# Kernel tuning notes

Hardware: AMD Instinct MI355X
Metric: run time of the kernel (lower is better)

Reference implementation:

```python
import jax, jax.numpy as jnp
import numpy as np

N_NODES = 20000
N_EDGES = 320000
F_IN = 256      # num_features_mol
HIDDEN = 512    # hidden_size


def _glorot(key, shape):
    fan_in, fan_out = shape
    lim = jnp.sqrt(6.0 / (fan_in + fan_out)).astype(jnp.float32)
    return jax.random.uniform(key, shape, jnp.float32, -lim, lim)


def setup_inputs() -> dict:
    key = jax.random.key(0)
    ks = jax.random.split(key, 12)
    x = jax.random.normal(ks[0], (N_NODES, F_IN), jnp.float32)
    edge_index = jax.random.randint(ks[1], (2, N_EDGES), 0, N_NODES, dtype=jnp.int64)
    d1, d2, d3 = F_IN * 2, F_IN * 2, F_IN * 4  # 512, 512, 1024
    return {
        "x": x,
        "edge_index": edge_index,
        # SAGEConv layer i: lin_l (neighbor, with bias), lin_r (root, no bias)
        "Wl1": _glorot(ks[2], (F_IN, d1)), "bl1": jnp.zeros((d1,), jnp.float32),
        "Wr1": _glorot(ks[3], (F_IN, d1)),
        "Wl2": _glorot(ks[4], (d1, d2)), "bl2": jnp.zeros((d2,), jnp.float32),
        "Wr2": _glorot(ks[5], (d1, d2)),
        "Wl3": _glorot(ks[6], (d2, d3)), "bl3": jnp.zeros((d3,), jnp.float32),
        "Wr3": _glorot(ks[7], (d2, d3)),
        # mol_fc_g1: Linear(4*F -> hidden)
        "Wfc": _glorot(ks[8], (d3, HIDDEN)), "bfc": jnp.zeros((HIDDEN,), jnp.float32),
    }


def _sage_mean(x, src, dst, Wl, bl, Wr):
    # mean-aggregate neighbor features: messages flow src -> dst
    msg = x[src]                                               # [E, d]
    agg = jax.ops.segment_sum(msg, dst, num_segments=N_NODES)  # [N, d]
    cnt = jax.ops.segment_sum(jnp.ones((src.shape[0],), x.dtype), dst,
                              num_segments=N_NODES)            # [N]
    mean = agg / jnp.maximum(cnt, 1.0)[:, None]                # zero-deg -> 0
    return mean @ Wl + bl + x @ Wr


def reference(x, edge_index, Wl1, bl1, Wr1, Wl2, bl2, Wr2, Wl3, bl3, Wr3, Wfc, bfc):
    src, dst = edge_index[0], edge_index[1]
    h = jax.nn.relu(_sage_mean(x, src, dst, Wl1, bl1, Wr1))
    h = jax.nn.relu(_sage_mean(h, src, dst, Wl2, bl2, Wr2))
    h = jax.nn.relu(_sage_mean(h, src, dst, Wl3, bl3, Wr3))
    return h @ Wfc + bfc                                       # [N, HIDDEN]
```

## Files before the change

### kernel.cpp

```cpp
#include <hip/hip_runtime.h>
#include <hip/hip_bf16.h>


typedef __bf16 bf16x8 __attribute__((ext_vector_type(8)));
typedef float  f32x4  __attribute__((ext_vector_type(4)));

#define N_NODES 20000
#define N_EDGES 320000
#define MPAD 20096

__device__ __forceinline__ int clampi(int v, int lo, int hi) {
    return v < lo ? lo : (v > hi ? hi : v);
}

__device__ __forceinline__ void load16_lds(const void* g, void* l) {
    __builtin_amdgcn_global_load_lds(
        (const __attribute__((address_space(1))) void*)g,
        (__attribute__((address_space(3))) void*)l, 16, 0, 0);
}


struct TDesc { const float* W; __bf16* Wt; int K, N, KT, koff, tile0; };
struct TDescs { TDesc d[7]; };

__global__ void k_prep(TDescs ds, const float* __restrict__ x,
                       __bf16* __restrict__ xrm, __bf16* __restrict__ acat,
                       const int* __restrict__ ei, int* __restrict__ cnt) {
    __shared__ float tile[32][33];
    int b = blockIdx.x;
    int tid = threadIdx.y * 32 + threadIdx.x;

    if (b < 2304) {
        int di = 0;
#pragma unroll
        for (int i = 1; i < 7; ++i)
            if (b >= ds.d[i].tile0) di = i;
        const float* W = ds.d[di].W;
        __bf16* Wt = ds.d[di].Wt;
        int N = ds.d[di].N, KT = ds.d[di].KT, koff = ds.d[di].koff;
        int t = b - ds.d[di].tile0;
        int ntn = N >> 5;
        int nb = (t % ntn) * 32, kb = (t / ntn) * 32;
        for (int i = 0; i < 32; i += 8) {
            int k = kb + threadIdx.y + i, n = nb + threadIdx.x;
            tile[threadIdx.y + i][threadIdx.x] = W[(size_t)k * N + n];
        }
        __syncthreads();
        for (int i = 0; i < 32; i += 8) {
            int n = nb + threadIdx.y + i, k = koff + kb + threadIdx.x;
            size_t o = (size_t)(n >> 7) * ((size_t)KT * 128) + (size_t)(k >> 3) * 1024 +
                       (size_t)((n & 127) * 8) + (k & 7);
            Wt[o] = (__bf16)tile[threadIdx.x][threadIdx.y + i];
        }
    } else if (b < 4804) {
        int node = (b - 2304) * 8 + (tid >> 5);
        int f0 = (tid & 31) * 8;
        float4 u = *(const float4*)(x + (size_t)node * 256 + f0);
        float4 w = *(const float4*)(x + (size_t)node * 256 + f0 + 4);
        alignas(16) __bf16 tmp[8] = {(__bf16)u.x, (__bf16)u.y, (__bf16)u.z, (__bf16)u.w,
                                     (__bf16)w.x, (__bf16)w.y, (__bf16)w.z, (__bf16)w.w};
        *(uint4*)(xrm + (size_t)node * 256 + f0) = *(const uint4*)tmp;
        *(uint4*)(acat + (size_t)(node >> 7) * (512 * 128) +
                  (size_t)(32 + (f0 >> 3)) * 1024 + (size_t)((node & 127) * 8)) =
            *(const uint4*)tmp;
    } else {
        int e = (b - 4804) * 256 + tid;
        atomicAdd(&cnt[clampi(ei[N_EDGES + e], 0, N_NODES - 1)], 1);
    }
}


__global__ __launch_bounds__(1024) void k_scan(const int* __restrict__ cnt,
                                               int* __restrict__ off,
                                               int* __restrict__ cur, int n) {
    __shared__ int sm[1024];
    __shared__ int carry;
    int tid = threadIdx.x;
    if (tid == 0) carry = 0;
    __syncthreads();
    for (int base = 0; base < n; base += 1024) {
        int i = base + tid;
        int v = (i < n) ? cnt[i] : 0;
        sm[tid] = v;
        __syncthreads();
        for (int s = 1; s < 1024; s <<= 1) {
            int t = (tid >= s) ? sm[tid - s] : 0;
            __syncthreads();
            sm[tid] += t;
            __syncthreads();
        }
        int exc = carry + sm[tid] - v;
        if (i < n) { off[i] = exc; cur[i] = exc; }
        __syncthreads();
        if (tid == 1023) carry += sm[1023];
        __syncthreads();
    }
    if (tid == 0) off[n] = carry;
}

__global__ void k_fill(const int* __restrict__ ei, int E,
                       int* __restrict__ cur, int* __restrict__ csr) {
    int e = blockIdx.x * blockDim.x + threadIdx.x;
    if (e < E) {
        int dst = clampi(ei[E + e], 0, N_NODES - 1);
        int src = clampi(ei[e], 0, N_NODES - 1);
        int pos = atomicAdd(&cur[dst], 1);
        if (pos >= 0 && pos < E) csr[pos] = src;
    }
}


template <int D, int KC>
__global__ __launch_bounds__(256) void k_agg(const __hip_bfloat16* __restrict__ hrm,
                                             const int* __restrict__ off,
                                             const int* __restrict__ csr,
                                             __bf16* __restrict__ acat) {
    constexpr int FPL = D / 64;
    int wave = threadIdx.x >> 6, lane = threadIdx.x & 63;
    int node = blockIdx.x * 4 + wave;
    int c0 = lane * FPL;
    int beg = off[node], end = off[node + 1];
    float a[FPL] = {};

    if constexpr (FPL == 8) {
        auto ldrow = [&](int s) { return *(const uint4*)(hrm + (size_t)s * D + c0); };
        auto addv = [&](uint4 v) {
            const __hip_bfloat16* hb = (const __hip_bfloat16*)&v;
#pragma unroll
            for (int j = 0; j < 8; ++j) a[j] += __bfloat162float(hb[j]);
        };
        int e = beg;
        for (; e + 3 < end; e += 4) {
            int s0 = csr[e], s1 = csr[e + 1], s2 = csr[e + 2], s3 = csr[e + 3];
            uint4 v0 = ldrow(s0), v1 = ldrow(s1), v2 = ldrow(s2), v3 = ldrow(s3);
            addv(v0); addv(v1); addv(v2); addv(v3);
        }
        for (; e < end; ++e) addv(ldrow(csr[e]));
    } else {
        auto ldrow = [&](int s) { return *(const uint2*)(hrm + (size_t)s * D + c0); };
        auto addv = [&](uint2 v) {
            const __hip_bfloat16* hb = (const __hip_bfloat16*)&v;
#pragma unroll
            for (int j = 0; j < 4; ++j) a[j] += __bfloat162float(hb[j]);
        };
        int e = beg;
        for (; e + 3 < end; e += 4) {
            int s0 = csr[e], s1 = csr[e + 1], s2 = csr[e + 2], s3 = csr[e + 3];
            uint2 v0 = ldrow(s0), v1 = ldrow(s1), v2 = ldrow(s2), v3 = ldrow(s3);
            addv(v0); addv(v1); addv(v2); addv(v3);
        }
        for (; e < end; ++e) addv(ldrow(csr[e]));
    }

    float inv = 1.f / fmaxf((float)(end - beg), 1.f);
    alignas(16) __bf16 tmp[FPL];
#pragma unroll
    for (int j = 0; j < FPL; ++j) tmp[j] = (__bf16)(a[j] * inv);

    __bf16* base = acat + (size_t)(node >> 7) * ((size_t)KC * 128) +
                   (size_t)((node & 127) * 8);
    if constexpr (FPL == 8) {
        *(uint4*)(base + (size_t)lane * 1024) = *(const uint4*)tmp;
    } else {
        *(uint2*)(base + (size_t)(lane >> 1) * 1024 + (size_t)((lane & 1) * 4)) =
            *(const uint2*)tmp;
    }
}


template <bool RELU, int OUTMODE>
__global__ __launch_bounds__(256) void k_gemm(const __bf16* __restrict__ A, int K, int M,
                                              const __bf16* __restrict__ B,
                                              const float* __restrict__ bias,
                                              __bf16* __restrict__ osw, int Kc, int coff,
                                              __bf16* __restrict__ orm, int ldrm,
                                              float* __restrict__ of32, int ldf,
                                              int rtiles, int ctlog2) {
    constexpr int SMEM = (OUTMODE == 2) ? 34816 : 32768;
    __shared__ char smem[SMEM];
    __bf16* Alds = (__bf16*)smem;
    __bf16* Blds = (__bf16*)(smem + 16384);

    int bid = blockIdx.x;
    int xcd = bid & 7, local = bid >> 3;
    int cmask = (1 << ctlog2) - 1;
    int colTile = local & cmask;
    int rowTile = (local >> ctlog2) * 8 + xcd;
    if (rowTile >= rtiles) return;

    const __bf16* Atile = A + (size_t)rowTile * ((size_t)K * 128);
    const __bf16* Btile = B + (size_t)colTile * ((size_t)K * 128);

    int tid = threadIdx.x;
    int wave = tid >> 6, lane = tid & 63;
    int wr = wave >> 1, wc = wave & 1;
    int quad = lane >> 4, l16 = lane & 15;

    f32x4 acc[4][4] = {};

    for (int k0 = 0; k0 < K; k0 += 64) {
        __syncthreads();
        const __bf16* gA = Atile + (size_t)k0 * 128;
        const __bf16* gB = Btile + (size_t)k0 * 128;
#pragma unroll
        for (int j = 0; j < 4; ++j) {
            int slot = (j * 256 + tid) * 8;
            load16_lds(gA + slot, Alds + slot);
            load16_lds(gB + slot, Blds + slot);
        }
        __syncthreads();
#pragma unroll
        for (int sp = 0; sp < 2; ++sp) {
            bf16x8 af[4], bf[4];
#pragma unroll
            for (int mi = 0; mi < 4; ++mi)
                af[mi] = *(const bf16x8*)(Alds + sp * 4096 + quad * 1024 +
                                          (wr * 64 + mi * 16 + l16) * 8);
#pragma unroll
            for (int ni = 0; ni < 4; ++ni)
                bf[ni] = *(const bf16x8*)(Blds + sp * 4096 + quad * 1024 +
                                          (wc * 64 + ni * 16 + l16) * 8);
#pragma unroll
            for (int mi = 0; mi < 4; ++mi)
#pragma unroll
                for (int ni = 0; ni < 4; ++ni)
                    acc[mi][ni] = __builtin_amdgcn_mfma_f32_16x16x32_bf16(
                        af[mi], bf[ni], acc[mi][ni], 0, 0, 0);
        }
    }

    int col0 = colTile * 128;
    int row0 = rowTile * 128;
    __syncthreads();

    if (OUTMODE != 2) {
        __bf16* cb = (__bf16*)smem;
#pragma unroll
        for (int ni = 0; ni < 4; ++ni) {
            int ct = wc * 64 + ni * 16 + l16;
            float bv = bias[col0 + ct];
#pragma unroll
            for (int mi = 0; mi < 4; ++mi) {
                int rb = wr * 64 + mi * 16 + quad * 4;
#pragma unroll
                for (int r = 0; r < 4; ++r) {
                    float v = acc[mi][ni][r] + bv;
                    if (RELU) v = fmaxf(v, 0.f);
                    cb[(ct >> 3) * 1024 + (rb + r) * 8 + (ct & 7)] = (__bf16)v;
                }
            }
        }
        __syncthreads();
        __bf16* dst = osw + (size_t)rowTile * ((size_t)Kc * 128) +
                      (size_t)((coff + col0) >> 3) * 1024;
#pragma unroll
        for (int p2 = 0; p2 < 8; ++p2) {
            int idx = (p2 * 256 + tid) * 8;
            *(uint4*)(dst + idx) = *(const uint4*)(cb + idx);
        }
        if (OUTMODE == 1) {
#pragma unroll
            for (int p2 = 0; p2 < 8; ++p2) {
                int rr = p2 * 16 + (tid >> 4);
                int cc = tid & 15;
                *(uint4*)(orm + (size_t)(row0 + rr) * ldrm + col0 + cc * 8) =
                    *(const uint4*)(cb + cc * 1024 + rr * 8);
            }
        }
    } else {
        float* cf = (float*)smem;
#pragma unroll
        for (int h = 0; h < 2; ++h) {
            if (wc == h) {
#pragma unroll
                for (int ni = 0; ni < 4; ++ni) {
                    int ctl = ni * 16 + l16;
                    float bv = bias[col0 + h * 64 + ctl];
#pragma unroll
                    for (int mi = 0; mi < 4; ++mi) {
                        int rb = wr * 64 + mi * 16 + quad * 4;
#pragma unroll
                        for (int r = 0; r < 4; ++r) {
                            float v = acc[mi][ni][r] + bv;
                            if (RELU) v = fmaxf(v, 0.f);
                            cf[(rb + r) * 68 + ctl] = v;
                        }
                    }
                }
            }
            __syncthreads();
            int chunk = tid & 15, rl = tid >> 4;
#pragma unroll
            for (int p2 = 0; p2 < 8; ++p2) {
                int rt = p2 * 16 + rl;
                int row = row0 + rt;
                if (row < M) {
                    float4 v = *(const float4*)(cf + rt * 68 + chunk * 4);
                    *(float4*)(of32 + (size_t)row * ldf + col0 + h * 64 + chunk * 4) = v;
                }
            }
            __syncthreads();
        }
    }
}


extern "C" void kernel_launch(void* const* d_in, const int* in_sizes, int n_in,
                              void* d_out, int out_size, void* d_ws, size_t ws_size,
                              hipStream_t stream) {
    const float* x   = (const float*)d_in[0];
    const int*   ei  = (const int*)d_in[1];
    const float* Wl1 = (const float*)d_in[2];
    const float* bl1 = (const float*)d_in[3];
    const float* Wr1 = (const float*)d_in[4];
    const float* Wl2 = (const float*)d_in[5];
    const float* bl2 = (const float*)d_in[6];
    const float* Wr2 = (const float*)d_in[7];
    const float* Wl3 = (const float*)d_in[8];
    const float* bl3 = (const float*)d_in[9];
    const float* Wr3 = (const float*)d_in[10];
    const float* Wfc = (const float*)d_in[11];
    const float* bfc = (const float*)d_in[12];
    float* out = (float*)d_out;

    const int NN = N_NODES, E = N_EDGES;

    char* p = (char*)d_ws;
    auto alloc = [&](size_t bytes) {
        char* r = p;
        p += (bytes + 511) & ~(size_t)511;
        return r;
    };
    int* cnt   = (int*)alloc((size_t)NN * 4);
    int* off   = (int*)alloc((size_t)(NN + 1) * 4);
    int* cur   = (int*)alloc((size_t)NN * 4);
    int* csr   = (int*)alloc((size_t)E * 4);
    __bf16* Acat1 = (__bf16*)alloc((size_t)MPAD * 512 * 2);
    __bf16* Acat2 = (__bf16*)alloc((size_t)MPAD * 1024 * 2);
    __bf16* Acat3 = (__bf16*)alloc((size_t)MPAD * 1024 * 2);
    __bf16* Hrm   = (__bf16*)alloc((size_t)MPAD * 512 * 2);
    __bf16* Xrm   = (__bf16*)alloc((size_t)MPAD * 256 * 2);
    __bf16* Wt1 = (__bf16*)alloc((size_t)512 * 512 * 2);
    __bf16* Wt2 = (__bf16*)alloc((size_t)512 * 1024 * 2);
    __bf16* Wt3 = (__bf16*)alloc((size_t)1024 * 1024 * 2);
    __bf16* Wt4 = (__bf16*)alloc((size_t)512 * 1024 * 2);
    __bf16* H3 = Acat2;

    hipMemsetAsync(cnt, 0, (size_t)NN * 4, stream);
    TDescs td;
    td.d[0] = {Wl1, Wt1, 256, 512, 512, 0, 0};
    td.d[1] = {Wr1, Wt1, 256, 512, 512, 256, 128};
    td.d[2] = {Wl2, Wt2, 512, 512, 1024, 0, 256};
    td.d[3] = {Wr2, Wt2, 512, 512, 1024, 512, 512};
    td.d[4] = {Wl3, Wt3, 512, 1024, 1024, 0, 768};
    td.d[5] = {Wr3, Wt3, 512, 1024, 1024, 512, 1280};
    td.d[6] = {Wfc, Wt4, 1024, 512, 1024, 0, 1792};
    k_prep<<<6054, dim3(32, 8), 0, stream>>>(td, x, Xrm, Acat1, ei, cnt);

    k_scan<<<1, 1024, 0, stream>>>(cnt, off, cur, NN);
    k_fill<<<(E + 255) / 256, 256, 0, stream>>>(ei, E, cur, csr);

    int rtiles = (NN + 127) / 128;
    int rg = ((rtiles + 7) / 8) * 8;

    k_agg<256, 512><<<NN / 4, 256, 0, stream>>>(
        (const __hip_bfloat16*)Xrm, off, csr, Acat1);
    k_gemm<true, 1><<<rg * 4, 256, 0, stream>>>(
        Acat1, 512, NN, Wt1, bl1, Acat2, 1024, 512, Hrm, 512, nullptr, 0, rtiles, 2);

    k_agg<512, 1024><<<NN / 4, 256, 0, stream>>>(
        (const __hip_bfloat16*)Hrm, off, csr, Acat2);
    k_gemm<true, 1><<<rg * 4, 256, 0, stream>>>(
        Acat2, 1024, NN, Wt2, bl2, Acat3, 1024, 512, Hrm, 512, nullptr, 0, rtiles, 2);

    k_agg<512, 1024><<<NN / 4, 256, 0, stream>>>(
        (const __hip_bfloat16*)Hrm, off, csr, Acat3);
    k_gemm<true, 0><<<rg * 8, 256, 0, stream>>>(
        Acat3, 1024, NN, Wt3, bl3, H3, 1024, 0, nullptr, 0, nullptr, 0, rtiles, 3);

    k_gemm<false, 2><<<rg * 4, 256, 0, stream>>>(
        H3, 1024, NN, Wt4, bfc, nullptr, 0, 0, nullptr, 0, out, 512, rtiles, 2);
}
```

Baseline: 443.4 us.

## Double-buffer GEMM LDS tiles and parallelize CSR offset scan across blocks

The GEMM main loop now uses two LDS buffers, so the global-to-LDS load of the next K tile is issued while MFMAs run on the current one, and one barrier per iteration is dropped. The single-block serial prefix scan over node counts is replaced by a three-kernel scan: a per-block scan, a serial carry over about 20 block sums, and a carry add. Doubling shared memory to 64KB per block may cut GEMM occupancy, and the scan now costs two extra kernel launches.

```diff
diff --git a/kernel.cpp b/kernel.cpp
--- a/kernel.cpp
+++ b/kernel.cpp
@@ -70,32 +70,43 @@
 }
 
 
-__global__ __launch_bounds__(1024) void k_scan(const int* __restrict__ cnt,
-                                               int* __restrict__ off,
-                                               int* __restrict__ cur, int n) {
+__global__ __launch_bounds__(1024) void k_scan_block(const int* __restrict__ cnt,
+                                                     int* __restrict__ off,
+                                                     int* __restrict__ bsum, int n) {
     __shared__ int sm[1024];
-    __shared__ int carry;
-    int tid = threadIdx.x;
-    if (tid == 0) carry = 0;
+    int b = blockIdx.x, tid = threadIdx.x;
+    int i = b * 1024 + tid;
+    int v = (i < n) ? cnt[i] : 0;
+    sm[tid] = v;
     __syncthreads();
-    for (int base = 0; base < n; base += 1024) {
-        int i = base + tid;
-        int v = (i < n) ? cnt[i] : 0;
-        sm[tid] = v;
+    for (int s = 1; s < 1024; s <<= 1) {
+        int t = (tid >= s) ? sm[tid - s] : 0;
         __syncthreads();
-        for (int s = 1; s < 1024; s <<= 1) {
-            int t = (tid >= s) ? sm[tid - s] : 0;
-            __syncthreads();
-            sm[tid] += t;
-            __syncthreads();
-        }
-        int exc = carry + sm[tid] - v;
-        if (i < n) { off[i] = exc; cur[i] = exc; }
+        sm[tid] += t;
         __syncthreads();
-        if (tid == 1023) carry += sm[1023];
-        __syncthreads();
-    }
-    if (tid == 0) off[n] = carry;
+    }
+    if (i < n) off[i] = sm[tid] - v;
+    if (tid == 1023) bsum[b] = sm[1023];
+}
+
+__global__ void k_scan_carry(const int* __restrict__ bsum, int* __restrict__ carry,
+                             int nb, int* __restrict__ off, int n) {
+    if (threadIdx.x == 0 && blockIdx.x == 0) {
+        int acc = 0;
+        for (int b = 0; b < nb; ++b) { carry[b] = acc; acc += bsum[b]; }
+        off[n] = acc;
+    }
+}
+
+__global__ __launch_bounds__(1024) void k_scan_add(int* __restrict__ off,
+                                                   int* __restrict__ cur,
+                                                   const int* __restrict__ carry, int n) {
+    int i = blockIdx.x * 1024 + threadIdx.x;
+    if (i < n) {
+        int v = off[i] + carry[blockIdx.x];
+        off[i] = v;
+        cur[i] = v;
+    }
 }
 
 __global__ void k_fill(const int* __restrict__ ei, int E,
@@ -176,10 +187,7 @@
                                               __bf16* __restrict__ orm, int ldrm,
                                               float* __restrict__ of32, int ldf,
                                               int rtiles, int ctlog2) {
-    constexpr int SMEM = (OUTMODE == 2) ? 34816 : 32768;
-    __shared__ char smem[SMEM];
-    __bf16* Alds = (__bf16*)smem;
-    __bf16* Blds = (__bf16*)(smem + 16384);
+    __shared__ char smem[65536];
 
     int bid = blockIdx.x;
     int xcd = bid & 7, local = bid >> 3;
@@ -197,18 +205,28 @@
     int quad = lane >> 4, l16 = lane & 15;
 
     f32x4 acc[4][4] = {};
-
-    for (int k0 = 0; k0 < K; k0 += 64) {
-        __syncthreads();
-        const __bf16* gA = Atile + (size_t)k0 * 128;
-        const __bf16* gB = Btile + (size_t)k0 * 128;
+    const int nt = K >> 6;
+
+    auto stage = [&](int buf, int t) {
+        const __bf16* gA = Atile + (size_t)t * 64 * 128;
+        const __bf16* gB = Btile + (size_t)t * 64 * 128;
+        __bf16* Al = (__bf16*)(smem + buf * 32768);
+        __bf16* Bl = Al + 8192;
 #pragma unroll
         for (int j = 0; j < 4; ++j) {
             int slot = (j * 256 + tid) * 8;
-            load16_lds(gA + slot, Alds + slot);
-            load16_lds(gB + slot, Blds + slot);
-        }
-        __syncthreads();
+            load16_lds(gA + slot, Al + slot);
+            load16_lds(gB + slot, Bl + slot);
+        }
+    };
+
+    stage(0, 0);
+    __syncthreads();
+    int cur = 0;
+    for (int t = 0; t < nt; ++t) {
+        if (t + 1 < nt) stage(cur ^ 1, t + 1);
+        const __bf16* Alds = (const __bf16*)(smem + cur * 32768);
+        const __bf16* Blds = Alds + 8192;
 #pragma unroll
         for (int sp = 0; sp < 2; ++sp) {
             bf16x8 af[4], bf[4];
@@ -227,11 +245,12 @@
                     acc[mi][ni] = __builtin_amdgcn_mfma_f32_16x16x32_bf16(
                         af[mi], bf[ni], acc[mi][ni], 0, 0, 0);
         }
+        __syncthreads();
+        cur ^= 1;
     }
 
     int col0 = colTile * 128;
     int row0 = rowTile * 128;
-    __syncthreads();
 
     if (OUTMODE != 2) {
         __bf16* cb = (__bf16*)smem;
@@ -324,6 +343,7 @@
     float* out = (float*)d_out;
 
     const int NN = N_NODES, E = N_EDGES;
+    const int NB = (NN + 1023) / 1024;
 
     char* p = (char*)d_ws;
     auto alloc = [&](size_t bytes) {
@@ -335,6 +355,8 @@
     int* off   = (int*)alloc((size_t)(NN + 1) * 4);
     int* cur   = (int*)alloc((size_t)NN * 4);
     int* csr   = (int*)alloc((size_t)E * 4);
+    int* bsum  = (int*)alloc((size_t)NB * 4);
+    int* carry = (int*)alloc((size_t)NB * 4);
     __bf16* Acat1 = (__bf16*)alloc((size_t)MPAD * 512 * 2);
     __bf16* Acat2 = (__bf16*)alloc((size_t)MPAD * 1024 * 2);
     __bf16* Acat3 = (__bf16*)alloc((size_t)MPAD * 1024 * 2);
@@ -357,7 +379,9 @@
     td.d[6] = {Wfc, Wt4, 1024, 512, 1024, 0, 1792};
     k_prep<<<6054, dim3(32, 8), 0, stream>>>(td, x, Xrm, Acat1, ei, cnt);
 
-    k_scan<<<1, 1024, 0, stream>>>(cnt, off, cur, NN);
+    k_scan_block<<<NB, 1024, 0, stream>>>(cnt, off, bsum, NN);
+    k_scan_carry<<<1, 64, 0, stream>>>(bsum, carry, NB, off, NN);
+    k_scan_add<<<NB, 1024, 0, stream>>>(off, cur, carry, NN);
     k_fill<<<(E + 255) / 256, 256, 0, stream>>>(ei, E, cur, csr);
 
     int rtiles = (NN + 127) / 128;
```

Measured after the change: 404.4 us. 8.8% less time.
